# Kernel tuning notes

Hardware: AMD Instinct MI355X
Metric: run time of the kernel (lower is better)

The kernel has to match this reference:

```python
import jax, jax.numpy as jnp
import numpy as np

N = 50000
E = 400000
NFEAT = 256
NHID = 64
HEADS = [4, 4, 4]
NCLASS = 121
NEG_SLOPE = 0.2


def gat_conv(h, W, al, ar, src, dst, H, D):
    # h: [N, F_in], W: [F_in, H*D], al/ar: [H, D]
    feat = (h @ W).reshape(N, H, D)                    # [N, H, D]
    el = jnp.sum(feat * al[None], axis=-1)             # [N, H]
    er = jnp.sum(feat * ar[None], axis=-1)             # [N, H]
    e = jax.nn.leaky_relu(el[src] + er[dst], NEG_SLOPE)  # [E, H]
    # edge softmax over incoming edges of each dst node
    m = jax.ops.segment_max(e, dst, num_segments=N)    # [N, H]
    ex = jnp.exp(e - m[dst])                           # [E, H]
    s = jax.ops.segment_sum(ex, dst, num_segments=N)   # [N, H]
    alpha = ex / s[dst]                                # [E, H]
    msg = alpha[..., None] * feat[src]                 # [E, H, D]
    return jax.ops.segment_sum(msg, dst, num_segments=N)  # [N, H, D]


def setup_inputs() -> dict:
    key = jax.random.key(0)
    ks = jax.random.split(key, 12)
    d = {
        "h": jax.random.normal(ks[0], (N, NFEAT), dtype=jnp.float32),
        "src": jax.random.randint(ks[1], (E,), 0, N),
        "dst": jax.random.randint(ks[2], (E,), 0, N),
        "W1": jax.random.normal(ks[3], (NFEAT, HEADS[0] * NHID), dtype=jnp.float32) * 0.05,
        "al1": jax.random.normal(ks[4], (HEADS[0], NHID), dtype=jnp.float32) * 0.1,
        "ar1": jax.random.normal(ks[5], (HEADS[0], NHID), dtype=jnp.float32) * 0.1,
        "W2": jax.random.normal(ks[6], (HEADS[0] * NHID, HEADS[1] * NHID), dtype=jnp.float32) * 0.05,
        "al2": jax.random.normal(ks[7], (HEADS[1], NHID), dtype=jnp.float32) * 0.1,
        "ar2": jax.random.normal(ks[8], (HEADS[1], NHID), dtype=jnp.float32) * 0.1,
        "W3": jax.random.normal(ks[9], (HEADS[1] * NHID, HEADS[2] * NCLASS), dtype=jnp.float32) * 0.05,
        "al3": jax.random.normal(ks[10], (HEADS[2], NCLASS), dtype=jnp.float32) * 0.1,
        "ar3": jax.random.normal(ks[11], (HEADS[2], NCLASS), dtype=jnp.float32) * 0.1,
    }
    return d


def reference(h, src, dst, W1, al1, ar1, W2, al2, ar2, W3, al3, ar3):
    # layer 1: [N, H0, NHID] -> flatten -> ELU (norm='none', drop=0, residual='none')
    x = gat_conv(h, W1, al1, ar1, src, dst, HEADS[0], NHID).reshape(N, -1)
    x = jax.nn.elu(x)
    # layer 2
    x = gat_conv(x, W2, al2, ar2, src, dst, HEADS[1], NHID).reshape(N, -1)
    x = jax.nn.elu(x)
    # output layer: mean over heads
    x = gat_conv(x, W3, al3, ar3, src, dst, HEADS[2], NCLASS).mean(axis=1)
    return x
```

## Files before the change

kernel.cpp:

```cpp
#include <hip/hip_runtime.h>
#include <cstddef>

#define NN 50000
#define NE 400000
#define NH 4
#define NC 121
#define MAXSLOT 600000

typedef __attribute__((ext_vector_type(8))) short short8;
typedef __attribute__((ext_vector_type(4))) float f32x4;
typedef __attribute__((ext_vector_type(2))) float f32x2;

static __device__ __forceinline__ unsigned short f2bf(float f) {
    unsigned u = __float_as_uint(f);
    u += 0x7fffu + ((u >> 16) & 1u);
    return (unsigned short)(u >> 16);
}
static __device__ __forceinline__ float bf2f(unsigned short u) {
    return __uint_as_float(((unsigned)u) << 16);
}
static __device__ __forceinline__ f32x2 bfpair(unsigned u) {
    f32x2 r;
    r.x = __uint_as_float(u << 16);
    r.y = __uint_as_float(u & 0xffff0000u);
    return r;
}
static __device__ __forceinline__ void load_lds16(const unsigned short* g, unsigned short* l) {
    __builtin_amdgcn_global_load_lds(
        (const __attribute__((address_space(1))) unsigned*)g,
        (__attribute__((address_space(3))) unsigned*)l, 16, 0, 0);
}

#define PREP_X    3200000
#define PREP_BT1  (PREP_X + 65536)
#define PREP_BT2  (PREP_BT1 + 65536)
#define PREP_CAT  (PREP_BT2 + 131072)
#define PREP_WV   (PREP_CAT + 2048)
#define PREP_END  (PREP_WV + NE)
__global__ __launch_bounds__(256) void prep_k(const float* __restrict__ h,
                                              const float* __restrict__ W1,
                                              const float* __restrict__ W2,
                                              const float* __restrict__ W3,
                                              const float* __restrict__ al3,
                                              const float* __restrict__ ar3,
                                              const int* __restrict__ dst,
                                              unsigned short* __restrict__ h_bf,
                                              unsigned short* __restrict__ BT1,
                                              unsigned short* __restrict__ BT2,
                                              unsigned short* __restrict__ BTcat,
                                              float* __restrict__ wl3,
                                              float* __restrict__ wr3,
                                              int* __restrict__ deg) {
    int i = blockIdx.x * blockDim.x + threadIdx.x;
    if (i < PREP_X) {
        float4 v = *(const float4*)&h[(size_t)i * 4];
        ushort4 o;
        o.x = f2bf(v.x); o.y = f2bf(v.y); o.z = f2bf(v.z); o.w = f2bf(v.w);
        *(ushort4*)&h_bf[(size_t)i * 4] = o;
    } else if (i < PREP_BT1) {
        int j = i - PREP_X;
        int n = j >> 8, k = j & 255;
        BT1[j] = f2bf(W1[(size_t)k * 256 + n]);
    } else if (i < PREP_BT2) {
        int j = i - PREP_BT1;
        int n = j >> 8, k = j & 255;
        BT2[j] = f2bf(W2[(size_t)k * 256 + n]);
    } else if (i < PREP_CAT) {
        int j = i - PREP_BT2;
        int c = j >> 10, kk = j & 1023;
        int hh = kk >> 8, k = kk & 255;
        float v = (c < NC) ? 0.25f * W3[(size_t)k * 484 + hh * NC + c] : 0.f;
        BTcat[j] = f2bf(v);
    } else if (i < PREP_WV) {
        int j = (i - PREP_CAT) & 1023;
        int sel = (i - PREP_CAT) >> 10;
        int hh = j >> 8, k = j & 255;
        const float* a = sel ? ar3 : al3;
        const float* wrow = W3 + (size_t)k * 484 + hh * NC;
        const float* arow = a + hh * NC;
        float s = 0.f;
        for (int d = 0; d < NC; ++d) s += wrow[d] * arow[d];
        if (sel) wr3[j] = s; else wl3[j] = s;
    } else if (i < PREP_END) {
        atomicAdd(&deg[dst[i - PREP_WV]], 1);
    }
}

__global__ __launch_bounds__(256) void gemm_bf16(const unsigned short* __restrict__ A,
                                                 const unsigned short* __restrict__ BT,
                                                 float* __restrict__ Cf,
                                                 unsigned short* __restrict__ Cb,
                                                 const float* __restrict__ al,
                                                 const float* __restrict__ ar,
                                                 float* __restrict__ el,
                                                 float* __restrict__ er,
                                                 int M, int Nout, int K) {
    __shared__ __align__(16) unsigned short Alds[128 * 32];
    __shared__ __align__(16) unsigned short Blds[128 * 32];
    const int tid = threadIdx.x;
    const int wave = tid >> 6;
    const int lane = tid & 63;
    const int quad = lane >> 4;
    const int ml = lane & 15;
    const int m0 = blockIdx.x * 128;
    const int n0 = blockIdx.y * 128;
    const int wm0 = (wave >> 1) * 64;
    const int wn0 = (wave & 1) * 64;

    const unsigned short* Ab = A + (size_t)(m0 + wave * 16 + (lane >> 2)) * K + (lane & 3) * 8;
    const unsigned short* Bb = BT + (size_t)(n0 + wave * 16 + (lane >> 2)) * K + (lane & 3) * 8;
    unsigned short* AldsW = Alds + wave * 512;
    unsigned short* BldsW = Blds + wave * 512;

    f32x4 acc[4][4] = {};

    for (int k0 = 0; k0 < K; k0 += 32) {
        #pragma unroll
        for (int p = 0; p < 2; ++p) {
            load_lds16(Ab + (size_t)(p * 64) * K + k0, AldsW + p * 2048);
            load_lds16(Bb + (size_t)(p * 64) * K + k0, BldsW + p * 2048);
        }
        __syncthreads();

        short8 af[4], bf[4];
        #pragma unroll
        for (int i = 0; i < 4; ++i)
            af[i] = *(const short8*)&Alds[(wm0 + i * 16 + ml) * 32 + quad * 8];
        #pragma unroll
        for (int j = 0; j < 4; ++j)
            bf[j] = *(const short8*)&Blds[(wn0 + j * 16 + ml) * 32 + quad * 8];
        #pragma unroll
        for (int i = 0; i < 4; ++i)
            #pragma unroll
            for (int j = 0; j < 4; ++j)
                acc[i][j] = __builtin_amdgcn_mfma_f32_16x16x32_bf16(af[i], bf[j], acc[i][j], 0, 0, 0);
        __syncthreads();
    }

    #pragma unroll
    for (int i = 0; i < 4; ++i) {
        #pragma unroll
        for (int reg = 0; reg < 4; ++reg) {
            int m = m0 + wm0 + i * 16 + quad * 4 + reg;
            if (m >= M) continue;
            #pragma unroll
            for (int j = 0; j < 4; ++j) {
                int n = n0 + wn0 + j * 16 + ml;
                if (n < Nout) {
                    if (Cb) Cb[(size_t)m * Nout + n] = f2bf(acc[i][j][reg]);
                    else    Cf[(size_t)m * Nout + n] = acc[i][j][reg];
                }
            }
        }
    }

    if (el) {
        int head = (n0 + wn0) >> 6;
        float alv[4], arv[4];
        #pragma unroll
        for (int j = 0; j < 4; ++j) {
            alv[j] = al[head * 64 + j * 16 + ml];
            arv[j] = ar[head * 64 + j * 16 + ml];
        }
        #pragma unroll
        for (int i = 0; i < 4; ++i) {
            #pragma unroll
            for (int reg = 0; reg < 4; ++reg) {
                float sl = 0.f, sr = 0.f;
                #pragma unroll
                for (int j = 0; j < 4; ++j) {
                    float v = acc[i][j][reg];
                    sl += v * alv[j];
                    sr += v * arv[j];
                }
                #pragma unroll
                for (int off = 1; off < 16; off <<= 1) {
                    sl += __shfl_xor(sl, off);
                    sr += __shfl_xor(sr, off);
                }
                int m = m0 + wm0 + i * 16 + quad * 4 + reg;
                if (ml == 0 && m < M) {
                    el[m * 4 + head] = sl;
                    er[m * 4 + head] = sr;
                }
            }
        }
    }
}

__global__ __launch_bounds__(256) void scan1(const int* __restrict__ deg,
                                             int* __restrict__ excl,
                                             int* __restrict__ partials) {
    __shared__ int sh[256];
    int i = blockIdx.x * 256 + threadIdx.x;
    int v = (i < NN) ? ((deg[i] + 3) & ~3) : 0;
    sh[threadIdx.x] = v;
    __syncthreads();
    for (int off = 1; off < 256; off <<= 1) {
        int t = (threadIdx.x >= off) ? sh[threadIdx.x - off] : 0;
        __syncthreads();
        sh[threadIdx.x] += t;
        __syncthreads();
    }
    if (i < NN) excl[i] = sh[threadIdx.x] - v;
    if (threadIdx.x == 255) partials[blockIdx.x] = sh[255];
}

__global__ __launch_bounds__(256) void scan2(int* __restrict__ partials, int nb) {
    __shared__ int sh[256];
    int t = threadIdx.x;
    int v = (t < nb) ? partials[t] : 0;
    sh[t] = v;
    __syncthreads();
    for (int off = 1; off < 256; off <<= 1) {
        int x = (t >= off) ? sh[t - off] : 0;
        __syncthreads();
        sh[t] += x;
        __syncthreads();
    }
    if (t < nb) partials[t] = sh[t] - v;
}

__global__ __launch_bounds__(256) void scan3(const int* __restrict__ excl,
                                             const int* __restrict__ partials,
                                             int* __restrict__ rowptr) {
    int i = blockIdx.x * 256 + threadIdx.x;
    if (i < NN) rowptr[i] = excl[i] + partials[blockIdx.x];
}

__global__ __launch_bounds__(256) void scatter_k(const int* __restrict__ src,
                                                 const int* __restrict__ dst,
                                                 const int* __restrict__ rowptr,
                                                 int* __restrict__ cursor,
                                                 int* __restrict__ ssrc,
                                                 int* __restrict__ sdst) {
    int e = blockIdx.x * blockDim.x + threadIdx.x;
    if (e >= NE) return;
    int d = dst[e];
    int p = atomicAdd(&cursor[d], 1);
    int pos = rowptr[d] + p;
    ssrc[pos] = src[e] << 9;
    sdst[pos] = d;
}

__global__ __launch_bounds__(256) void edgew_k(const int* __restrict__ ssrc,
                                               const int* __restrict__ sdst,
                                               const float* __restrict__ el,
                                               const float* __restrict__ er,
                                               float* __restrict__ wcsr) {
    int i = blockIdx.x * blockDim.x + threadIdx.x;
    if (i >= MAXSLOT) return;
    int d = sdst[i];
    float w0 = 0.f, w1 = 0.f, w2 = 0.f, w3 = 0.f;
    if (d >= 0) {
        int su = ssrc[i];
        float4 e_l = *(const float4*)((const char*)el + (su >> 5));
        float4 e_r = *(const float4*)&er[d * 4];
        float v0 = e_l.x + e_r.x; v0 = fmaxf(v0, 0.2f * v0);
        float v1 = e_l.y + e_r.y; v1 = fmaxf(v1, 0.2f * v1);
        float v2 = e_l.z + e_r.z; v2 = fmaxf(v2, 0.2f * v2);
        float v3 = e_l.w + e_r.w; v3 = fmaxf(v3, 0.2f * v3);
        w0 = __expf(v0); w1 = __expf(v1); w2 = __expf(v2); w3 = __expf(v3);
    }
    wcsr[0 * MAXSLOT + i] = w0;
    wcsr[1 * MAXSLOT + i] = w1;
    wcsr[2 * MAXSLOT + i] = w2;
    wcsr[3 * MAXSLOT + i] = w3;
}

__global__ __launch_bounds__(256) void agg256(const int* __restrict__ rowptr,
                                              const int* __restrict__ deg,
                                              const int* __restrict__ ssrc,
                                              const float* __restrict__ el,
                                              const float* __restrict__ er,
                                              const unsigned short* __restrict__ feat,
                                              unsigned short* __restrict__ ybf,
                                              const float* __restrict__ wl3,
                                              const float* __restrict__ wr3,
                                              float* __restrict__ el3,
                                              float* __restrict__ er3) {
    int wid = (blockIdx.x * blockDim.x + threadIdx.x) >> 6;
    int lane = threadIdx.x & 63;
    if (wid >= NN) return;
    int n = wid;
    int start = rowptr[n];
    int cnt = deg[n];
    int cnt4 = (cnt + 3) & ~3;
    int head = lane >> 4;
    float ern = er[n * 4 + head];
    const char* elb = (const char*)el + head * 4;
    const char* fbase = (const char*)feat + lane * 8;
    f32x2 a01 = {0.f, 0.f}, a23 = {0.f, 0.f};
    float ssum = 0.f;
    for (int k = 0; k < cnt4; k += 4) {
        int4 sv = *(const int4*)&ssrc[start + k];
        float e0 = *(const float*)(elb + (sv.x >> 5));
        float e1 = *(const float*)(elb + (sv.y >> 5));
        float e2 = *(const float*)(elb + (sv.z >> 5));
        float e3 = *(const float*)(elb + (sv.w >> 5));
        float v0 = e0 + ern; v0 = fmaxf(v0, 0.2f * v0);
        float v1 = e1 + ern; v1 = fmaxf(v1, 0.2f * v1);
        float v2 = e2 + ern; v2 = fmaxf(v2, 0.2f * v2);
        float v3 = e3 + ern; v3 = fmaxf(v3, 0.2f * v3);
        float w0 = (k + 0 < cnt) ? __expf(v0) : 0.f;
        float w1 = (k + 1 < cnt) ? __expf(v1) : 0.f;
        float w2 = (k + 2 < cnt) ? __expf(v2) : 0.f;
        float w3 = (k + 3 < cnt) ? __expf(v3) : 0.f;
        uint2 u0 = *(const uint2*)(fbase + sv.x);
        uint2 u1 = *(const uint2*)(fbase + sv.y);
        uint2 u2 = *(const uint2*)(fbase + sv.z);
        uint2 u3 = *(const uint2*)(fbase + sv.w);
        ssum += (w0 + w1) + (w2 + w3);
        a01 += w0 * bfpair(u0.x); a23 += w0 * bfpair(u0.y);
        a01 += w1 * bfpair(u1.x); a23 += w1 * bfpair(u1.y);
        a01 += w2 * bfpair(u2.x); a23 += w2 * bfpair(u2.y);
        a01 += w3 * bfpair(u3.x); a23 += w3 * bfpair(u3.y);
    }
    float inv = ssum > 0.f ? 1.0f / ssum : 0.f;
    float r0 = a01.x * inv, r1 = a01.y * inv, r2 = a23.x * inv, r3 = a23.y * inv;
    r0 = r0 > 0.f ? r0 : (__expf(r0) - 1.f);
    r1 = r1 > 0.f ? r1 : (__expf(r1) - 1.f);
    r2 = r2 > 0.f ? r2 : (__expf(r2) - 1.f);
    r3 = r3 > 0.f ? r3 : (__expf(r3) - 1.f);
    ushort4 o;
    o.x = f2bf(r0); o.y = f2bf(r1); o.z = f2bf(r2); o.w = f2bf(r3);
    *(ushort4*)&ybf[(size_t)n * 256 + lane * 4] = o;

    if (wl3) {
        float sl[4], sr[4];
        #pragma unroll
        for (int h = 0; h < 4; ++h) {
            float4 a4 = *(const float4*)&wl3[h * 256 + lane * 4];
            float4 b4 = *(const float4*)&wr3[h * 256 + lane * 4];
            sl[h] = r0 * a4.x + r1 * a4.y + r2 * a4.z + r3 * a4.w;
            sr[h] = r0 * b4.x + r1 * b4.y + r2 * b4.z + r3 * b4.w;
        }
        #pragma unroll
        for (int off = 32; off; off >>= 1) {
            #pragma unroll
            for (int h = 0; h < 4; ++h) {
                sl[h] += __shfl_xor(sl[h], off);
                sr[h] += __shfl_xor(sr[h], off);
            }
        }
        if (lane == 0) {
            #pragma unroll
            for (int h = 0; h < 4; ++h) {
                el3[n * 4 + h] = sl[h];
                er3[n * 4 + h] = sr[h];
            }
        }
    }
}

__global__ __launch_bounds__(256) void agg3(const int* __restrict__ rowptr,
                                            const int* __restrict__ deg,
                                            const int* __restrict__ ssrc,
                                            const float* __restrict__ wcsr,
                                            const unsigned short* __restrict__ x,
                                            unsigned short* __restrict__ xagg) {
    int wid = (blockIdx.x * blockDim.x + threadIdx.x) >> 6;
    int lane = threadIdx.x & 63;
    if (wid >= NN) return;
    int n = wid;
    int start = rowptr[n];
    int cnt4 = (deg[n] + 3) & ~3;
    const char* xbase = (const char*)x + lane * 8;
    f32x2 accA[4] = {}, accB[4] = {};
    float ssum[4] = {};
    for (int k = 0; k < cnt4; k += 4) {
        int4 sv = *(const int4*)&ssrc[start + k];
        float4 w0 = *(const float4*)&wcsr[0 * MAXSLOT + start + k];
        float4 w1 = *(const float4*)&wcsr[1 * MAXSLOT + start + k];
        float4 w2 = *(const float4*)&wcsr[2 * MAXSLOT + start + k];
        float4 w3 = *(const float4*)&wcsr[3 * MAXSLOT + start + k];
        uint2 u0 = *(const uint2*)(xbase + sv.x);
        uint2 u1 = *(const uint2*)(xbase + sv.y);
        uint2 u2 = *(const uint2*)(xbase + sv.z);
        uint2 u3 = *(const uint2*)(xbase + sv.w);
        ssum[0] += (w0.x + w0.y) + (w0.z + w0.w);
        ssum[1] += (w1.x + w1.y) + (w1.z + w1.w);
        ssum[2] += (w2.x + w2.y) + (w2.z + w2.w);
        ssum[3] += (w3.x + w3.y) + (w3.z + w3.w);
        f32x2 fa = bfpair(u0.x), fA = bfpair(u0.y);
        f32x2 fb = bfpair(u1.x), fB = bfpair(u1.y);
        f32x2 fc = bfpair(u2.x), fC = bfpair(u2.y);
        f32x2 fd = bfpair(u3.x), fD = bfpair(u3.y);
        accA[0] += w0.x * fa + w0.y * fb + w0.z * fc + w0.w * fd;
        accB[0] += w0.x * fA + w0.y * fB + w0.z * fC + w0.w * fD;
        accA[1] += w1.x * fa + w1.y * fb + w1.z * fc + w1.w * fd;
        accB[1] += w1.x * fA + w1.y * fB + w1.z * fC + w1.w * fD;
        accA[2] += w2.x * fa + w2.y * fb + w2.z * fc + w2.w * fd;
        accB[2] += w2.x * fA + w2.y * fB + w2.z * fC + w2.w * fD;
        accA[3] += w3.x * fa + w3.y * fb + w3.z * fc + w3.w * fd;
        accB[3] += w3.x * fA + w3.y * fB + w3.z * fC + w3.w * fD;
    }
    #pragma unroll
    for (int h = 0; h < 4; ++h) {
        float inv = ssum[h] > 0.f ? 1.f / ssum[h] : 0.f;
        ushort4 o;
        o.x = f2bf(accA[h].x * inv); o.y = f2bf(accA[h].y * inv);
        o.z = f2bf(accB[h].x * inv); o.w = f2bf(accB[h].y * inv);
        *(ushort4*)&xagg[(size_t)n * 1024 + h * 256 + lane * 4] = o;
    }
}

extern "C" void kernel_launch(void* const* d_in, const int* in_sizes, int n_in,
                              void* d_out, int out_size, void* d_ws, size_t ws_size,
                              hipStream_t stream) {
    const float* h   = (const float*)d_in[0];
    const int*   src = (const int*)d_in[1];
    const int*   dst = (const int*)d_in[2];
    const float* W1  = (const float*)d_in[3];
    const float* al1 = (const float*)d_in[4];
    const float* ar1 = (const float*)d_in[5];
    const float* W2  = (const float*)d_in[6];
    const float* al2 = (const float*)d_in[7];
    const float* ar2 = (const float*)d_in[8];
    const float* W3  = (const float*)d_in[9];
    const float* al3 = (const float*)d_in[10];
    const float* ar3 = (const float*)d_in[11];
    float* out = (float*)d_out;

    float* ws = (float*)d_ws;
    unsigned short* x_bf    = (unsigned short*)ws;
    unsigned short* h_bf    = (unsigned short*)(ws + 6400000);
    unsigned short* feat_bf = (unsigned short*)(ws + 12800000);
    unsigned short* xagg    = (unsigned short*)(ws + 6400000);
    float* el  = ws + 32000000;
    float* er  = ws + 32200000;
    float* wl3 = ws + 32400000;
    float* wr3 = ws + 32401024;
    unsigned short* BT1   = (unsigned short*)(ws + 32402048);
    unsigned short* BT2   = (unsigned short*)(ws + 32434816);
    unsigned short* BTcat = (unsigned short*)(ws + 32467584);
    float* wcsr = ws + 32533120;
    int* ibase  = (int*)(ws + 34933120);
    int* deg      = ibase;
    int* cursor   = ibase + 50000;
    int* excl     = ibase + 100000;
    int* partials = ibase + 150000;
    int* rowptr   = ibase + 150256;
    int* ssrc     = ibase + 200256;
    int* sdst     = ibase + 800256;
    float* el2 = ws + 36333376;
    float* er2 = ws + 36533376;

    const int NB = (NN + 255) / 256;
    const int SLOT_BLOCKS = (MAXSLOT + 255) / 256;

    hipMemsetAsync(deg, 0, 2 * NN * sizeof(int), stream);
    hipMemsetAsync(ssrc, 0, MAXSLOT * sizeof(int), stream);
    hipMemsetAsync(sdst, 0xFF, MAXSLOT * sizeof(int), stream);

    prep_k<<<(PREP_END + 255) / 256, 256, 0, stream>>>(h, W1, W2, W3, al3, ar3, dst,
                                                       h_bf, BT1, BT2, BTcat, wl3, wr3, deg);

    scan1<<<NB, 256, 0, stream>>>(deg, excl, partials);
    scan2<<<1, 256, 0, stream>>>(partials, NB);
    scan3<<<NB, 256, 0, stream>>>(excl, partials, rowptr);
    scatter_k<<<(NE + 255) / 256, 256, 0, stream>>>(src, dst, rowptr, cursor, ssrc, sdst);

    dim3 g256((NN + 127) / 128, 2);
    dim3 gOut((NN + 127) / 128, 1);
    const int WAVE_BLOCKS = (NN * 64 + 255) / 256;

    gemm_bf16<<<g256, 256, 0, stream>>>(h_bf, BT1, nullptr, feat_bf, al1, ar1, el, er, NN, 256, 256);
    agg256<<<WAVE_BLOCKS, 256, 0, stream>>>(rowptr, deg, ssrc, el, er, feat_bf, x_bf,
                                            nullptr, nullptr, nullptr, nullptr);

    gemm_bf16<<<g256, 256, 0, stream>>>(x_bf, BT2, nullptr, feat_bf, al2, ar2, el, er, NN, 256, 256);
    agg256<<<WAVE_BLOCKS, 256, 0, stream>>>(rowptr, deg, ssrc, el, er, feat_bf, x_bf,
                                            wl3, wr3, el2, er2);

    edgew_k<<<SLOT_BLOCKS, 256, 0, stream>>>(ssrc, sdst, el2, er2, wcsr);
    agg3<<<WAVE_BLOCKS, 256, 0, stream>>>(rowptr, deg, ssrc, wcsr, x_bf, xagg);
    gemm_bf16<<<gOut, 256, 0, stream>>>(xagg, BTcat, out, nullptr, nullptr, nullptr, nullptr, nullptr, NN, NC, 1024);
}
```

Measured before the change: 405.8 us.

## Reorder output layer to project first then aggregate, fusing edge weights

Output layer previously aggregated 1024-wide per-head inputs and then ran a GEMM. It now projects x with a padded 4x128 weight (512 columns) first, then aggregates per-head 128-wide bf16 features with edge softmax weights computed inline, reducing across heads with shuffles. This removes the edge-weight kernel, the sdst array and its memset, and halves gathered row width. In exchange the GEMM output widens, there is a per-head exp per lane, and masking relies on the padded slot count.

```diff
diff --git a/kernel.cpp b/kernel.cpp
--- a/kernel.cpp
+++ b/kernel.cpp
@@ -47,7 +47,7 @@
                                               unsigned short* __restrict__ h_bf,
                                               unsigned short* __restrict__ BT1,
                                               unsigned short* __restrict__ BT2,
-                                              unsigned short* __restrict__ BTcat,
+                                              unsigned short* __restrict__ BT3,
                                               float* __restrict__ wl3,
                                               float* __restrict__ wr3,
                                               int* __restrict__ deg) {
@@ -67,10 +67,10 @@
         BT2[j] = f2bf(W2[(size_t)k * 256 + n]);
     } else if (i < PREP_CAT) {
         int j = i - PREP_BT2;
-        int c = j >> 10, kk = j & 1023;
-        int hh = kk >> 8, k = kk & 255;
+        int np = j >> 8, k = j & 255;
+        int hh = np >> 7, c = np & 127;
         float v = (c < NC) ? 0.25f * W3[(size_t)k * 484 + hh * NC + c] : 0.f;
-        BTcat[j] = f2bf(v);
+        BT3[j] = f2bf(v);
     } else if (i < PREP_WV) {
         int j = (i - PREP_CAT) & 1023;
         int sel = (i - PREP_CAT) >> 10;
@@ -232,40 +232,13 @@
                                                  const int* __restrict__ dst,
                                                  const int* __restrict__ rowptr,
                                                  int* __restrict__ cursor,
-                                                 int* __restrict__ ssrc,
-                                                 int* __restrict__ sdst) {
+                                                 int* __restrict__ ssrc) {
     int e = blockIdx.x * blockDim.x + threadIdx.x;
     if (e >= NE) return;
     int d = dst[e];
     int p = atomicAdd(&cursor[d], 1);
     int pos = rowptr[d] + p;
     ssrc[pos] = src[e] << 9;
-    sdst[pos] = d;
-}
-
-__global__ __launch_bounds__(256) void edgew_k(const int* __restrict__ ssrc,
-                                               const int* __restrict__ sdst,
-                                               const float* __restrict__ el,
-                                               const float* __restrict__ er,
-                                               float* __restrict__ wcsr) {
-    int i = blockIdx.x * blockDim.x + threadIdx.x;
-    if (i >= MAXSLOT) return;
-    int d = sdst[i];
-    float w0 = 0.f, w1 = 0.f, w2 = 0.f, w3 = 0.f;
-    if (d >= 0) {
-        int su = ssrc[i];
-        float4 e_l = *(const float4*)((const char*)el + (su >> 5));
-        float4 e_r = *(const float4*)&er[d * 4];
-        float v0 = e_l.x + e_r.x; v0 = fmaxf(v0, 0.2f * v0);
-        float v1 = e_l.y + e_r.y; v1 = fmaxf(v1, 0.2f * v1);
-        float v2 = e_l.z + e_r.z; v2 = fmaxf(v2, 0.2f * v2);
-        float v3 = e_l.w + e_r.w; v3 = fmaxf(v3, 0.2f * v3);
-        w0 = __expf(v0); w1 = __expf(v1); w2 = __expf(v2); w3 = __expf(v3);
-    }
-    wcsr[0 * MAXSLOT + i] = w0;
-    wcsr[1 * MAXSLOT + i] = w1;
-    wcsr[2 * MAXSLOT + i] = w2;
-    wcsr[3 * MAXSLOT + i] = w3;
 }
 
 __global__ __launch_bounds__(256) void agg256(const int* __restrict__ rowptr,
@@ -353,55 +326,67 @@
     }
 }
 
-__global__ __launch_bounds__(256) void agg3(const int* __restrict__ rowptr,
-                                            const int* __restrict__ deg,
-                                            const int* __restrict__ ssrc,
-                                            const float* __restrict__ wcsr,
-                                            const unsigned short* __restrict__ x,
-                                            unsigned short* __restrict__ xagg) {
+__global__ __launch_bounds__(256) void agg3f(const int* __restrict__ rowptr,
+                                             const int* __restrict__ deg,
+                                             const int* __restrict__ ssrc,
+                                             const float* __restrict__ el,
+                                             const float* __restrict__ er,
+                                             const unsigned short* __restrict__ feat3,
+                                             float* __restrict__ out) {
     int wid = (blockIdx.x * blockDim.x + threadIdx.x) >> 6;
     int lane = threadIdx.x & 63;
     if (wid >= NN) return;
     int n = wid;
     int start = rowptr[n];
-    int cnt4 = (deg[n] + 3) & ~3;
-    const char* xbase = (const char*)x + lane * 8;
-    f32x2 accA[4] = {}, accB[4] = {};
-    float ssum[4] = {};
+    int cnt = deg[n];
+    int cnt4 = (cnt + 3) & ~3;
+    int head = lane >> 4;
+    float ern = er[n * 4 + head];
+    const char* elb = (const char*)el + head * 4;
+    const char* fbase = (const char*)feat3 + lane * 16;
+    f32x2 acc[4] = {};
+    float ssum = 0.f;
     for (int k = 0; k < cnt4; k += 4) {
         int4 sv = *(const int4*)&ssrc[start + k];
-        float4 w0 = *(const float4*)&wcsr[0 * MAXSLOT + start + k];
-        float4 w1 = *(const float4*)&wcsr[1 * MAXSLOT + start + k];
-        float4 w2 = *(const float4*)&wcsr[2 * MAXSLOT + start + k];
-        float4 w3 = *(const float4*)&wcsr[3 * MAXSLOT + start + k];
-        uint2 u0 = *(const uint2*)(xbase + sv.x);
-        uint2 u1 = *(const uint2*)(xbase + sv.y);
-        uint2 u2 = *(const uint2*)(xbase + sv.z);
-        uint2 u3 = *(const uint2*)(xbase + sv.w);
-        ssum[0] += (w0.x + w0.y) + (w0.z + w0.w);
-        ssum[1] += (w1.x + w1.y) + (w1.z + w1.w);
-        ssum[2] += (w2.x + w2.y) + (w2.z + w2.w);
-        ssum[3] += (w3.x + w3.y) + (w3.z + w3.w);
-        f32x2 fa = bfpair(u0.x), fA = bfpair(u0.y);
-        f32x2 fb = bfpair(u1.x), fB = bfpair(u1.y);
-        f32x2 fc = bfpair(u2.x), fC = bfpair(u2.y);
-        f32x2 fd = bfpair(u3.x), fD = bfpair(u3.y);
-        accA[0] += w0.x * fa + w0.y * fb + w0.z * fc + w0.w * fd;
-        accB[0] += w0.x * fA + w0.y * fB + w0.z * fC + w0.w * fD;
-        accA[1] += w1.x * fa + w1.y * fb + w1.z * fc + w1.w * fd;
-        accB[1] += w1.x * fA + w1.y * fB + w1.z * fC + w1.w * fD;
-        accA[2] += w2.x * fa + w2.y * fb + w2.z * fc + w2.w * fd;
-        accB[2] += w2.x * fA + w2.y * fB + w2.z * fC + w2.w * fD;
-        accA[3] += w3.x * fa + w3.y * fb + w3.z * fc + w3.w * fd;
-        accB[3] += w3.x * fA + w3.y * fB + w3.z * fC + w3.w * fD;
-    }
+        float e0 = *(const float*)(elb + (sv.x >> 5));
+        float e1 = *(const float*)(elb + (sv.y >> 5));
+        float e2 = *(const float*)(elb + (sv.z >> 5));
+        float e3 = *(const float*)(elb + (sv.w >> 5));
+        uint4 u0 = *(const uint4*)(fbase + ((size_t)(unsigned)sv.x << 1));
+        uint4 u1 = *(const uint4*)(fbase + ((size_t)(unsigned)sv.y << 1));
+        uint4 u2 = *(const uint4*)(fbase + ((size_t)(unsigned)sv.z << 1));
+        uint4 u3 = *(const uint4*)(fbase + ((size_t)(unsigned)sv.w << 1));
+        float v0 = e0 + ern; v0 = fmaxf(v0, 0.2f * v0);
+        float v1 = e1 + ern; v1 = fmaxf(v1, 0.2f * v1);
+        float v2 = e2 + ern; v2 = fmaxf(v2, 0.2f * v2);
+        float v3 = e3 + ern; v3 = fmaxf(v3, 0.2f * v3);
+        float w0 = (k + 0 < cnt) ? __expf(v0) : 0.f;
+        float w1 = (k + 1 < cnt) ? __expf(v1) : 0.f;
+        float w2 = (k + 2 < cnt) ? __expf(v2) : 0.f;
+        float w3 = (k + 3 < cnt) ? __expf(v3) : 0.f;
+        ssum += (w0 + w1) + (w2 + w3);
+        acc[0] += w0 * bfpair(u0.x) + w1 * bfpair(u1.x) + w2 * bfpair(u2.x) + w3 * bfpair(u3.x);
+        acc[1] += w0 * bfpair(u0.y) + w1 * bfpair(u1.y) + w2 * bfpair(u2.y) + w3 * bfpair(u3.y);
+        acc[2] += w0 * bfpair(u0.z) + w1 * bfpair(u1.z) + w2 * bfpair(u2.z) + w3 * bfpair(u3.z);
+        acc[3] += w0 * bfpair(u0.w) + w1 * bfpair(u1.w) + w2 * bfpair(u2.w) + w3 * bfpair(u3.w);
+    }
+    float iv = ssum > 0.f ? 1.f / ssum : 0.f;
+    float r[8];
+    r[0] = acc[0].x * iv; r[1] = acc[0].y * iv;
+    r[2] = acc[1].x * iv; r[3] = acc[1].y * iv;
+    r[4] = acc[2].x * iv; r[5] = acc[2].y * iv;
+    r[6] = acc[3].x * iv; r[7] = acc[3].y * iv;
     #pragma unroll
-    for (int h = 0; h < 4; ++h) {
-        float inv = ssum[h] > 0.f ? 1.f / ssum[h] : 0.f;
-        ushort4 o;
-        o.x = f2bf(accA[h].x * inv); o.y = f2bf(accA[h].y * inv);
-        o.z = f2bf(accB[h].x * inv); o.w = f2bf(accB[h].y * inv);
-        *(ushort4*)&xagg[(size_t)n * 1024 + h * 256 + lane * 4] = o;
+    for (int j = 0; j < 8; ++j) {
+        r[j] += __shfl_xor(r[j], 16);
+        r[j] += __shfl_xor(r[j], 32);
+    }
+    if (lane < 16) {
+        int c0 = lane * 8;
+        float* ob = out + (size_t)n * NC + c0;
+        #pragma unroll
+        for (int j = 0; j < 8; ++j)
+            if (c0 + j < NC) ob[j] = r[j];
     }
 }
 
@@ -426,15 +411,14 @@
     unsigned short* x_bf    = (unsigned short*)ws;
     unsigned short* h_bf    = (unsigned short*)(ws + 6400000);
     unsigned short* feat_bf = (unsigned short*)(ws + 12800000);
-    unsigned short* xagg    = (unsigned short*)(ws + 6400000);
+    unsigned short* feat3   = (unsigned short*)(ws + 6400000);
     float* el  = ws + 32000000;
     float* er  = ws + 32200000;
     float* wl3 = ws + 32400000;
     float* wr3 = ws + 32401024;
-    unsigned short* BT1   = (unsigned short*)(ws + 32402048);
-    unsigned short* BT2   = (unsigned short*)(ws + 32434816);
-    unsigned short* BTcat = (unsigned short*)(ws + 32467584);
-    float* wcsr = ws + 32533120;
+    unsigned short* BT1 = (unsigned short*)(ws + 32402048);
+    unsigned short* BT2 = (unsigned short*)(ws + 32434816);
+    unsigned short* BT3 = (unsigned short*)(ws + 32467584);
     int* ibase  = (int*)(ws + 34933120);
     int* deg      = ibase;
     int* cursor   = ibase + 50000;
@@ -442,27 +426,23 @@
     int* partials = ibase + 150000;
     int* rowptr   = ibase + 150256;
     int* ssrc     = ibase + 200256;
-    int* sdst     = ibase + 800256;
     float* el2 = ws + 36333376;
     float* er2 = ws + 36533376;
 
     const int NB = (NN + 255) / 256;
-    const int SLOT_BLOCKS = (MAXSLOT + 255) / 256;
 
     hipMemsetAsync(deg, 0, 2 * NN * sizeof(int), stream);
     hipMemsetAsync(ssrc, 0, MAXSLOT * sizeof(int), stream);
-    hipMemsetAsync(sdst, 0xFF, MAXSLOT * sizeof(int), stream);
 
     prep_k<<<(PREP_END + 255) / 256, 256, 0, stream>>>(h, W1, W2, W3, al3, ar3, dst,
-                                                       h_bf, BT1, BT2, BTcat, wl3, wr3, deg);
+                                                       h_bf, BT1, BT2, BT3, wl3, wr3, deg);
 
     scan1<<<NB, 256, 0, stream>>>(deg, excl, partials);
     scan2<<<1, 256, 0, stream>>>(partials, NB);
     scan3<<<NB, 256, 0, stream>>>(excl, partials, rowptr);
-    scatter_k<<<(NE + 255) / 256, 256, 0, stream>>>(src, dst, rowptr, cursor, ssrc, sdst);
+    scatter_k<<<(NE + 255) / 256, 256, 0, stream>>>(src, dst, rowptr, cursor, ssrc);
 
     dim3 g256((NN + 127) / 128, 2);
-    dim3 gOut((NN + 127) / 128, 1);
     const int WAVE_BLOCKS = (NN * 64 + 255) / 256;
 
     gemm_bf16<<<g256, 256, 0, stream>>>(h_bf, BT1, nullptr, feat_bf, al1, ar1, el, er, NN, 256, 256);
@@ -473,7 +453,8 @@
     agg256<<<WAVE_BLOCKS, 256, 0, stream>>>(rowptr, deg, ssrc, el, er, feat_bf, x_bf,
                                             wl3, wr3, el2, er2);
 
-    edgew_k<<<SLOT_BLOCKS, 256, 0, stream>>>(ssrc, sdst, el2, er2, wcsr);
-    agg3<<<WAVE_BLOCKS, 256, 0, stream>>>(rowptr, deg, ssrc, wcsr, x_bf, xagg);
-    gemm_bf16<<<gOut, 256, 0, stream>>>(xagg, BTcat, out, nullptr, nullptr, nullptr, nullptr, nullptr, NN, NC, 1024);
-}
+    gemm_bf16<<<dim3((NN + 127) / 128, 4), 256, 0, stream>>>(x_bf, BT3, nullptr, feat3,
+                                                             nullptr, nullptr, nullptr, nullptr,
+                                                             NN, 512, 256);
+    agg3f<<<WAVE_BLOCKS, 256, 0, stream>>>(rowptr, deg, ssrc, el2, er2, feat3, out);
+}
```

Result: no change. 409.3 us (+0.9%).

## Fuse layer-3 aggregation with output GEMM through shared memory

Applied to the files above, without the earlier changes.

Replaces the separate layer-3 aggregation kernel and the final bf16 GEMM with one kernel. Each block aggregates 16 nodes into a shared-memory tile of [16 x 1024] bf16 and then multiplies it by BTcat with MFMA to write the output directly. This removes the 100MB xagg write and re-read plus one launch. The cost is small 16-row MFMA tiles: each block reloads the B matrix from global memory, and there is less parallelism per wave, since each wave handles 4 nodes sequentially.

```diff
diff --git a/kernel.cpp b/kernel.cpp
--- a/kernel.cpp
+++ b/kernel.cpp
@@ -15,9 +15,6 @@
     unsigned u = __float_as_uint(f);
     u += 0x7fffu + ((u >> 16) & 1u);
     return (unsigned short)(u >> 16);
-}
-static __device__ __forceinline__ float bf2f(unsigned short u) {
-    return __uint_as_float(((unsigned)u) << 16);
 }
 static __device__ __forceinline__ f32x2 bfpair(unsigned u) {
     f32x2 r;
@@ -353,55 +350,89 @@
     }
 }
 
-__global__ __launch_bounds__(256) void agg3(const int* __restrict__ rowptr,
-                                            const int* __restrict__ deg,
-                                            const int* __restrict__ ssrc,
-                                            const float* __restrict__ wcsr,
-                                            const unsigned short* __restrict__ x,
-                                            unsigned short* __restrict__ xagg) {
-    int wid = (blockIdx.x * blockDim.x + threadIdx.x) >> 6;
-    int lane = threadIdx.x & 63;
-    if (wid >= NN) return;
-    int n = wid;
-    int start = rowptr[n];
-    int cnt4 = (deg[n] + 3) & ~3;
-    const char* xbase = (const char*)x + lane * 8;
-    f32x2 accA[4] = {}, accB[4] = {};
-    float ssum[4] = {};
-    for (int k = 0; k < cnt4; k += 4) {
-        int4 sv = *(const int4*)&ssrc[start + k];
-        float4 w0 = *(const float4*)&wcsr[0 * MAXSLOT + start + k];
-        float4 w1 = *(const float4*)&wcsr[1 * MAXSLOT + start + k];
-        float4 w2 = *(const float4*)&wcsr[2 * MAXSLOT + start + k];
-        float4 w3 = *(const float4*)&wcsr[3 * MAXSLOT + start + k];
-        uint2 u0 = *(const uint2*)(xbase + sv.x);
-        uint2 u1 = *(const uint2*)(xbase + sv.y);
-        uint2 u2 = *(const uint2*)(xbase + sv.z);
-        uint2 u3 = *(const uint2*)(xbase + sv.w);
-        ssum[0] += (w0.x + w0.y) + (w0.z + w0.w);
-        ssum[1] += (w1.x + w1.y) + (w1.z + w1.w);
-        ssum[2] += (w2.x + w2.y) + (w2.z + w2.w);
-        ssum[3] += (w3.x + w3.y) + (w3.z + w3.w);
-        f32x2 fa = bfpair(u0.x), fA = bfpair(u0.y);
-        f32x2 fb = bfpair(u1.x), fB = bfpair(u1.y);
-        f32x2 fc = bfpair(u2.x), fC = bfpair(u2.y);
-        f32x2 fd = bfpair(u3.x), fD = bfpair(u3.y);
-        accA[0] += w0.x * fa + w0.y * fb + w0.z * fc + w0.w * fd;
-        accB[0] += w0.x * fA + w0.y * fB + w0.z * fC + w0.w * fD;
-        accA[1] += w1.x * fa + w1.y * fb + w1.z * fc + w1.w * fd;
-        accB[1] += w1.x * fA + w1.y * fB + w1.z * fC + w1.w * fD;
-        accA[2] += w2.x * fa + w2.y * fb + w2.z * fc + w2.w * fd;
-        accB[2] += w2.x * fA + w2.y * fB + w2.z * fC + w2.w * fD;
-        accA[3] += w3.x * fa + w3.y * fb + w3.z * fc + w3.w * fd;
-        accB[3] += w3.x * fA + w3.y * fB + w3.z * fC + w3.w * fD;
+__global__ __launch_bounds__(256) void agg3m(const int* __restrict__ rowptr,
+                                             const int* __restrict__ deg,
+                                             const int* __restrict__ ssrc,
+                                             const float* __restrict__ wcsr,
+                                             const unsigned short* __restrict__ x,
+                                             const unsigned short* __restrict__ BTcat,
+                                             float* __restrict__ out) {
+    __shared__ __align__(16) unsigned short xlds[16 * 1032];
+    const int tid = threadIdx.x;
+    const int wave = tid >> 6;
+    const int lane = tid & 63;
+    const int nb0 = blockIdx.x * 16;
+    const char* fbase = (const char*)x + lane * 8;
+
+    for (int t = 0; t < 4; ++t) {
+        int nl = wave * 4 + t;
+        int n = nb0 + nl;
+        int start = rowptr[n];
+        int cnt4 = (deg[n] + 3) & ~3;
+        f32x2 accA[4] = {}, accB[4] = {};
+        float ssum[4] = {};
+        for (int k = 0; k < cnt4; k += 4) {
+            int4 sv = *(const int4*)&ssrc[start + k];
+            float4 w0 = *(const float4*)&wcsr[0 * MAXSLOT + start + k];
+            float4 w1 = *(const float4*)&wcsr[1 * MAXSLOT + start + k];
+            float4 w2 = *(const float4*)&wcsr[2 * MAXSLOT + start + k];
+            float4 w3 = *(const float4*)&wcsr[3 * MAXSLOT + start + k];
+            uint2 u0 = *(const uint2*)(fbase + sv.x);
+            uint2 u1 = *(const uint2*)(fbase + sv.y);
+            uint2 u2 = *(const uint2*)(fbase + sv.z);
+            uint2 u3 = *(const uint2*)(fbase + sv.w);
+            ssum[0] += (w0.x + w0.y) + (w0.z + w0.w);
+            ssum[1] += (w1.x + w1.y) + (w1.z + w1.w);
+            ssum[2] += (w2.x + w2.y) + (w2.z + w2.w);
+            ssum[3] += (w3.x + w3.y) + (w3.z + w3.w);
+            f32x2 fa = bfpair(u0.x), fA = bfpair(u0.y);
+            f32x2 fb = bfpair(u1.x), fB = bfpair(u1.y);
+            f32x2 fc = bfpair(u2.x), fC = bfpair(u2.y);
+            f32x2 fd = bfpair(u3.x), fD = bfpair(u3.y);
+            accA[0] += w0.x * fa + w0.y * fb + w0.z * fc + w0.w * fd;
+            accB[0] += w0.x * fA + w0.y * fB + w0.z * fC + w0.w * fD;
+            accA[1] += w1.x * fa + w1.y * fb + w1.z * fc + w1.w * fd;
+            accB[1] += w1.x * fA + w1.y * fB + w1.z * fC + w1.w * fD;
+            accA[2] += w2.x * fa + w2.y * fb + w2.z * fc + w2.w * fd;
+            accB[2] += w2.x * fA + w2.y * fB + w2.z * fC + w2.w * fD;
+            accA[3] += w3.x * fa + w3.y * fb + w3.z * fc + w3.w * fd;
+            accB[3] += w3.x * fA + w3.y * fB + w3.z * fC + w3.w * fD;
+        }
+        char* xrow = (char*)xlds + nl * 2064 + lane * 8;
+        #pragma unroll
+        for (int hh = 0; hh < 4; ++hh) {
+            float inv = ssum[hh] > 0.f ? 1.f / ssum[hh] : 0.f;
+            ushort4 o;
+            o.x = f2bf(accA[hh].x * inv); o.y = f2bf(accA[hh].y * inv);
+            o.z = f2bf(accB[hh].x * inv); o.w = f2bf(accB[hh].y * inv);
+            *(ushort4*)(xrow + hh * 512) = o;
+        }
+    }
+    __syncthreads();
+
+    const int ml = lane & 15;
+    const int quad = lane >> 4;
+    f32x4 acc[2] = {};
+    const char* albase = (const char*)xlds + ml * 2064 + quad * 16;
+    const unsigned short* Bb = BTcat + (size_t)(wave * 32 + ml) * 1024 + quad * 8;
+    #pragma unroll 4
+    for (int k0 = 0; k0 < 1024; k0 += 32) {
+        short8 af = *(const short8*)(albase + k0 * 2);
+        short8 b0 = *(const short8*)&Bb[k0];
+        short8 b1 = *(const short8*)&Bb[16 * 1024 + k0];
+        acc[0] = __builtin_amdgcn_mfma_f32_16x16x32_bf16(af, b0, acc[0], 0, 0, 0);
+        acc[1] = __builtin_amdgcn_mfma_f32_16x16x32_bf16(af, b1, acc[1], 0, 0, 0);
     }
     #pragma unroll
-    for (int h = 0; h < 4; ++h) {
-        float inv = ssum[h] > 0.f ? 1.f / ssum[h] : 0.f;
-        ushort4 o;
-        o.x = f2bf(accA[h].x * inv); o.y = f2bf(accA[h].y * inv);
-        o.z = f2bf(accB[h].x * inv); o.w = f2bf(accB[h].y * inv);
-        *(ushort4*)&xagg[(size_t)n * 1024 + h * 256 + lane * 4] = o;
+    for (int j = 0; j < 2; ++j) {
+        int col = wave * 32 + j * 16 + ml;
+        if (col < NC) {
+            #pragma unroll
+            for (int reg = 0; reg < 4; ++reg) {
+                int node = nb0 + quad * 4 + reg;
+                out[(size_t)node * NC + col] = acc[j][reg];
+            }
+        }
     }
 }
 
@@ -426,7 +457,6 @@
     unsigned short* x_bf    = (unsigned short*)ws;
     unsigned short* h_bf    = (unsigned short*)(ws + 6400000);
     unsigned short* feat_bf = (unsigned short*)(ws + 12800000);
-    unsigned short* xagg    = (unsigned short*)(ws + 6400000);
     float* el  = ws + 32000000;
     float* er  = ws + 32200000;
     float* wl3 = ws + 32400000;
@@ -462,7 +492,6 @@
     scatter_k<<<(NE + 255) / 256, 256, 0, stream>>>(src, dst, rowptr, cursor, ssrc, sdst);
 
     dim3 g256((NN + 127) / 128, 2);
-    dim3 gOut((NN + 127) / 128, 1);
     const int WAVE_BLOCKS = (NN * 64 + 255) / 256;
 
     gemm_bf16<<<g256, 256, 0, stream>>>(h_bf, BT1, nullptr, feat_bf, al1, ar1, el, er, NN, 256, 256);
@@ -474,6 +503,5 @@
                                             wl3, wr3, el2, er2);
 
     edgew_k<<<SLOT_BLOCKS, 256, 0, stream>>>(ssrc, sdst, el2, er2, wcsr);
-    agg3<<<WAVE_BLOCKS, 256, 0, stream>>>(rowptr, deg, ssrc, wcsr, x_bf, xagg);
-    gemm_bf16<<<gOut, 256, 0, stream>>>(xagg, BTcat, out, nullptr, nullptr, nullptr, nullptr, nullptr, NN, NC, 1024);
-}
+    agg3m<<<NN / 16, 256, 0, stream>>>(rowptr, deg, ssrc, wcsr, x_bf, BTcat, out);
+}
```

Result: slower. 454.0 us (+11.9%).
